# Kernel tuning notes

Measured on AMD Instinct MI355X. Metric: run time of the kernel, lower is better.

The kernel has to match this reference:

```python
import jax, jax.numpy as jnp
import numpy as np

C_IN, C_OUT, KH, KW = 64, 128, 3, 3
STRIDE, PAD, DIL = 1, 1, 1
EPS = 1e-5


def setup_inputs() -> dict:
    key = jax.random.key(0)
    ks = jax.random.split(key, 7)
    B, H, W = 8, 112, 112
    x = jax.random.normal(ks[0], (B, C_IN, H, W), dtype=jnp.float32)
    # offset conv: produces 2*KH*KW offset channels; small init keeps offsets sane
    w_off = jax.random.normal(ks[1], (2 * KH * KW, C_IN, KH, KW), dtype=jnp.float32) * 0.01
    b_off = jax.random.normal(ks[2], (2 * KH * KW,), dtype=jnp.float32) * 0.01
    # deformable conv weight/bias
    fan_in = C_IN * KH * KW
    w_dcn = jax.random.normal(ks[3], (C_OUT, C_IN, KH, KW), dtype=jnp.float32) / np.sqrt(fan_in)
    b_dcn = jax.random.normal(ks[4], (C_OUT,), dtype=jnp.float32) * 0.01
    gamma = jnp.ones((C_OUT,), dtype=jnp.float32)
    beta = jnp.zeros((C_OUT,), dtype=jnp.float32)
    return {"x": x, "w_off": w_off, "b_off": b_off, "w_dcn": w_dcn,
            "b_dcn": b_dcn, "gamma": gamma, "beta": beta}


def _conv2d(x, w, b):
    y = jax.lax.conv_general_dilated(
        x, w, window_strides=(STRIDE, STRIDE),
        padding=((PAD, PAD), (PAD, PAD)),
        rhs_dilation=(DIL, DIL),
        dimension_numbers=("NCHW", "OIHW", "NCHW"))
    return y + b[None, :, None, None]


def _deform_conv(x, offset, w, b):
    # x: [B,C,H,W]; offset: [B, 2*KH*KW, Ho, Wo] with (dy, dx) pairs per tap
    B, C, H, W = x.shape
    KK = KH * KW
    Ho, Wo = offset.shape[2], offset.shape[3]
    off = offset.reshape(B, KK, 2, Ho, Wo)
    ky = (jnp.arange(KK) // KW).astype(jnp.float32)  # kernel row per tap
    kx = (jnp.arange(KK) % KW).astype(jnp.float32)
    base_y = (jnp.arange(Ho) * STRIDE - PAD).astype(jnp.float32)
    base_x = (jnp.arange(Wo) * STRIDE - PAD).astype(jnp.float32)
    # sampling positions [B, KK, Ho, Wo]
    py = off[:, :, 0] + base_y[None, None, :, None] + (ky * DIL)[None, :, None, None]
    px = off[:, :, 1] + base_x[None, None, None, :] + (kx * DIL)[None, :, None, None]

    y0 = jnp.floor(py)
    x0 = jnp.floor(px)
    wy1 = py - y0  # weight for y0+1
    wx1 = px - x0
    y0i = y0.astype(jnp.int32)
    x0i = x0.astype(jnp.int32)

    x_flat = x.reshape(B, C, H * W)

    def gather_corner(yi, xi, wgt):
        # yi, xi, wgt: [B, KK, Ho, Wo]
        valid = (yi >= 0) & (yi < H) & (xi >= 0) & (xi < W)
        idx = jnp.clip(yi, 0, H - 1) * W + jnp.clip(xi, 0, W - 1)
        idx = idx.reshape(B, -1)  # [B, KK*Ho*Wo]
        vals = jnp.take_along_axis(x_flat, idx[:, None, :], axis=2)  # [B, C, N]
        coef = (wgt * valid.astype(wgt.dtype)).reshape(B, 1, -1)
        return vals * coef

    samp = (gather_corner(y0i,     x0i,     (1 - wy1) * (1 - wx1))
            + gather_corner(y0i,     x0i + 1, (1 - wy1) * wx1)
            + gather_corner(y0i + 1, x0i,     wy1 * (1 - wx1))
            + gather_corner(y0i + 1, x0i + 1, wy1 * wx1))
    samp = samp.reshape(B, C, KK, Ho, Wo)
    out = jnp.einsum("bckhw,ock->bohw", samp, w.reshape(w.shape[0], C, KK))
    return out + b[None, :, None, None]


def reference(x, w_off, b_off, w_dcn, b_dcn, gamma, beta):
    offset = _conv2d(x, w_off, b_off)
    y = _deform_conv(x, offset, w_dcn, b_dcn)
    # BatchNorm2d (training mode: biased batch stats) + ReLU
    mean = jnp.mean(y, axis=(0, 2, 3))
    var = jnp.var(y, axis=(0, 2, 3))
    yhat = (y - mean[None, :, None, None]) * jax.lax.rsqrt(var + EPS)[None, :, None, None]
    y = gamma[None, :, None, None] * yhat + beta[None, :, None, None]
    return jax.nn.relu(y)
```

## Files before the change

kernel.cpp:

```cpp
#include <hip/hip_runtime.h>

#define H    112
#define W    112
#define HW   12544
#define CIN  64
#define COUT 128
#define BATCH 8
#define KK   9
#define OFFC 18
#define EPS  1e-5f
#define TP   32
#define KDIM 576
#define KHALF 288
#define KPAD2 296
#define NB   3136
#define YST  40

typedef unsigned short ushort;
typedef unsigned int uint;
typedef __attribute__((ext_vector_type(8))) short short8;
typedef __attribute__((ext_vector_type(4))) float floatx4;
typedef __attribute__((ext_vector_type(2))) float f32x2;

__device__ __forceinline__ ushort f2bf(float f) {
  uint u = __float_as_uint(f);
  u = (u + 0x7FFFu + ((u >> 16) & 1u)) >> 16;
  return (ushort)u;
}

__device__ __forceinline__ uint pack_bf2(float f0, float f1) {
  uint u0 = __float_as_uint(f0) + 0x8000u;
  uint u1 = __float_as_uint(f1) + 0x8000u;
  return __builtin_amdgcn_perm(u1, u0, 0x07060302u);
}

__device__ __forceinline__ f32x2 up2(uint u) {
  f32x2 r;
  r.x = __uint_as_float(u << 16);
  r.y = __uint_as_float(u & 0xFFFF0000u);
  return r;
}

__global__ __launch_bounds__(256) void k_prep(
    const float* __restrict__ x, const float* __restrict__ w_off,
    const float* __restrict__ w_dcn, ushort* __restrict__ xTb,
    ushort* __restrict__ w_offT, ushort* __restrict__ w_mf) {
  if (blockIdx.y < BATCH) {
    __shared__ float tile[64][65];
    int b = blockIdx.y;
    int p0 = blockIdx.x * 64;
    int tid = threadIdx.x;
    int j = tid & 63, cb = tid >> 6;
#pragma unroll
    for (int i = 0; i < 16; ++i) {
      int ci = cb * 16 + i;
      tile[ci][j] = x[((size_t)(b * CIN + ci)) * HW + p0 + j];
    }
    __syncthreads();
    int px = tid >> 2, ciq = tid & 3;
#pragma unroll
    for (int g = 0; g < 4; ++g) {
      int ci = ciq * 16 + g * 4;
      uint lo = pack_bf2(tile[ci + 0][px], tile[ci + 1][px]);
      uint hi = pack_bf2(tile[ci + 2][px], tile[ci + 3][px]);
      *(uint2*)&xTb[((size_t)b * HW + p0 + px) * 64 + ci] = make_uint2(lo, hi);
    }
  } else {
    const int TOT = 32 * KDIM + COUT * KDIM;
    for (int i = blockIdx.x * 256 + threadIdx.x; i < TOT; i += 196 * 256) {
      if (i < 32 * KDIM) {
        int oc = i / KDIM, k = i - oc * KDIM;
        int kk = k >> 6, ci = k & 63;
        float v = (oc < OFFC) ? w_off[(oc * CIN + ci) * KK + kk] : 0.f;
        w_offT[i] = f2bf(v);
      } else {
        int jj = i - 32 * KDIM;
        int co = jj / KDIM, k = jj - co * KDIM;
        int h2 = k / KHALF, r = k - h2 * KHALF;
        int kk = r >> 5, cil = r & 31;
        int ci = h2 * 32 + cil;
        w_mf[jj] = f2bf(w_dcn[(co * CIN + ci) * KK + kk]);
      }
    }
  }
}

__global__ __launch_bounds__(256, 6) void k_deform(
    const ushort* __restrict__ xTb, const ushort* __restrict__ w_offT,
    const float* __restrict__ b_off, const ushort* __restrict__ w_mf,
    ushort* __restrict__ y, float* __restrict__ psT) {
  __shared__ float4  s_w[KK][TP];
  __shared__ ushort4 s_ip[KK][TP];
  __shared__ __align__(16) char smem_raw[TP * KPAD2 * 2];
  ushort (*samp)[KPAD2] = (ushort(*)[KPAD2])smem_raw;
  float  (*off_lds)[TP] = (float (*)[TP])smem_raw;

  int b = blockIdx.y;
  int p0 = blockIdx.x * TP;
  int bid = blockIdx.y * gridDim.x + blockIdx.x;
  int tid = threadIdx.x;
  const ushort* xb = xTb + (size_t)b * HW * 64;

  int wave = tid >> 6, lane = tid & 63;
  int row16 = lane & 15, quad = lane >> 4;

  {
    int pxblk = wave & 1, ocblk = wave >> 1;
    int pxl = pxblk * 16 + row16;
    int p = p0 + pxl;
    int ho = p / W, wo = p - ho * W;
    const ushort* wa = w_offT + (size_t)(ocblk * 16 + row16) * KDIM + quad * 8;
    floatx4 oacc = {0.f, 0.f, 0.f, 0.f};
#pragma unroll
    for (int ks = 0; ks < 18; ++ks) {
      int kk = ks >> 1;
      int ci0 = (ks & 1) * 32 + quad * 8;
      int kh = kk / 3, kw = kk - kh * 3;
      int yy = ho + kh - 1, xx = wo + kw - 1;
      short8 bv = {0, 0, 0, 0, 0, 0, 0, 0};
      if (yy >= 0 && yy < H && xx >= 0 && xx < W)
        bv = *(const short8*)(xb + ((size_t)(yy * W + xx) << 6) + ci0);
      short8 av = *(const short8*)(wa + ks * 32);
      oacc = __builtin_amdgcn_mfma_f32_16x16x32_bf16(av, bv, oacc, 0, 0, 0);
    }
#pragma unroll
    for (int reg = 0; reg < 4; ++reg) {
      int oc = ocblk * 16 + quad * 4 + reg;
      if (oc < OFFC) off_lds[oc][pxl] = oacc[reg] + b_off[oc];
    }
  }
  __syncthreads();

  for (int it = tid; it < KK * TP; it += 256) {
    int kk = it >> 5;
    int px = it & 31;
    int p = p0 + px;
    int ho = p / W, wo = p - ho * W;
    float dy = off_lds[2 * kk][px];
    float dx = off_lds[2 * kk + 1][px];
    float py = dy + (float)(ho - 1 + kk / 3);
    float pxx = dx + (float)(wo - 1 + kk % 3);
    float y0f = floorf(py), x0f = floorf(pxx);
    float wy1 = py - y0f, wx1 = pxx - x0f;
    int y0 = (int)y0f, x0 = (int)x0f;
    int y1 = y0 + 1, x1 = x0 + 1;
    float vy0 = (y0 >= 0 && y0 < H) ? 1.f : 0.f;
    float vy1 = (y1 >= 0 && y1 < H) ? 1.f : 0.f;
    float vx0 = (x0 >= 0 && x0 < W) ? 1.f : 0.f;
    float vx1 = (x1 >= 0 && x1 < W) ? 1.f : 0.f;
    int cy0 = min(max(y0, 0), H - 1), cy1 = min(max(y1, 0), H - 1);
    int cx0 = min(max(x0, 0), W - 1), cx1 = min(max(x1, 0), W - 1);
    s_w[kk][px] = make_float4((1.f - wy1) * (1.f - wx1) * vy0 * vx0,
                              (1.f - wy1) * wx1 * vy0 * vx1,
                              wy1 * (1.f - wx1) * vy1 * vx0,
                              wy1 * wx1 * vy1 * vx1);
    s_ip[kk][px] = make_ushort4((ushort)(cy0 * W + cx0), (ushort)(cy0 * W + cx1),
                                (ushort)(cy1 * W + cx0), (ushort)(cy1 * W + cx1));
  }
  __syncthreads();

  int koff = quad * 8;
  int co_base = wave * 32;
  const ushort* wa0 = w_mf + (size_t)(co_base + row16) * KDIM + koff;
  const ushort* wa1 = w_mf + (size_t)(co_base + 16 + row16) * KDIM + koff;

  floatx4 acc00 = {0.f, 0.f, 0.f, 0.f}, acc01 = acc00, acc10 = acc00, acc11 = acc00;

  for (int h = 0; h < 2; ++h) {
#pragma unroll
    for (int r = 0; r < 5; ++r) {
      int it = tid + r * 256;
      if (it < KK * TP * 4) {
        int kk = it >> 7;
        int px = (it >> 2) & 31;
        int cig = it & 3;
        int cil0 = cig * 8;
        int cio = h * 32 + cil0;
        float4 wv = s_w[kk][px];
        ushort4 ip = s_ip[kk][px];
        const ushort* g0 = xb + (((int)ip.x) << 6) + cio;
        const ushort* g1 = xb + (((int)ip.y) << 6) + cio;
        const ushort* g2 = xb + (((int)ip.z) << 6) + cio;
        const ushort* g3 = xb + (((int)ip.w) << 6) + cio;
        uint4 c0 = *(const uint4*)g0;
        uint4 c1 = *(const uint4*)g1;
        uint4 c2 = *(const uint4*)g2;
        uint4 c3 = *(const uint4*)g3;
        f32x2 r0 = up2(c0.x) * wv.x + up2(c1.x) * wv.y + up2(c2.x) * wv.z + up2(c3.x) * wv.w;
        f32x2 r1 = up2(c0.y) * wv.x + up2(c1.y) * wv.y + up2(c2.y) * wv.z + up2(c3.y) * wv.w;
        f32x2 r2 = up2(c0.z) * wv.x + up2(c1.z) * wv.y + up2(c2.z) * wv.z + up2(c3.z) * wv.w;
        f32x2 r3 = up2(c0.w) * wv.x + up2(c1.w) * wv.y + up2(c2.w) * wv.z + up2(c3.w) * wv.w;
        *(uint4*)&samp[px][kk * 32 + cil0] =
            make_uint4(pack_bf2(r0.x, r0.y), pack_bf2(r1.x, r1.y),
                       pack_bf2(r2.x, r2.y), pack_bf2(r3.x, r3.y));
      }
    }
    __syncthreads();

    const ushort* sb0 = &samp[row16][koff];
    const ushort* sb1 = &samp[16 + row16][koff];
    const ushort* a0 = wa0 + h * KHALF;
    const ushort* a1 = wa1 + h * KHALF;
#pragma unroll
    for (int ks = 0; ks < 9; ++ks) {
      short8 A0 = *(const short8*)(a0 + ks * 32);
      short8 A1 = *(const short8*)(a1 + ks * 32);
      short8 B0 = *(const short8*)(sb0 + ks * 32);
      short8 B1 = *(const short8*)(sb1 + ks * 32);
      acc00 = __builtin_amdgcn_mfma_f32_16x16x32_bf16(A0, B0, acc00, 0, 0, 0);
      acc01 = __builtin_amdgcn_mfma_f32_16x16x32_bf16(A0, B1, acc01, 0, 0, 0);
      acc10 = __builtin_amdgcn_mfma_f32_16x16x32_bf16(A1, B0, acc10, 0, 0, 0);
      acc11 = __builtin_amdgcn_mfma_f32_16x16x32_bf16(A1, B1, acc11, 0, 0, 0);
    }
    __syncthreads();
  }

  ushort (*yst)[YST] = (ushort(*)[YST])smem_raw;
#pragma unroll
  for (int reg = 0; reg < 4; ++reg) {
    int r0 = quad * 4 + reg;
    yst[co_base + r0][row16]            = f2bf(acc00[reg]);
    yst[co_base + r0][16 + row16]       = f2bf(acc01[reg]);
    yst[co_base + 16 + r0][row16]       = f2bf(acc10[reg]);
    yst[co_base + 16 + r0][16 + row16]  = f2bf(acc11[reg]);
  }
#pragma unroll
  for (int reg = 0; reg < 4; ++reg) {
    float s0 = acc00[reg] + acc01[reg];
    float q0 = acc00[reg] * acc00[reg] + acc01[reg] * acc01[reg];
    float s1 = acc10[reg] + acc11[reg];
    float q1 = acc10[reg] * acc10[reg] + acc11[reg] * acc11[reg];
#pragma unroll
    for (int m = 1; m < 16; m <<= 1) {
      s0 += __shfl_xor(s0, m, 64);
      q0 += __shfl_xor(q0, m, 64);
      s1 += __shfl_xor(s1, m, 64);
      q1 += __shfl_xor(q1, m, 64);
    }
    if (row16 == 0) {
      int c0 = co_base + quad * 4 + reg;
      float* pb = psT + (size_t)bid * 256;
      pb[c0] = s0;
      pb[COUT + c0] = q0;
      pb[c0 + 16] = s1;
      pb[COUT + c0 + 16] = q1;
    }
  }
  __syncthreads();
  {
    int co = tid >> 1, hf = tid & 1;
    const ushort* src = &yst[co][hf * 16];
    uint4 v0 = *(const uint4*)src;
    uint4 v1 = *(const uint4*)(src + 8);
    ushort* dst = y + (size_t)b * COUT * HW + (size_t)co * HW + p0 + hf * 16;
    *(uint4*)dst = v0;
    *(uint4*)(dst + 8) = v1;
  }
}

__global__ __launch_bounds__(256) void k_reduce(const float* __restrict__ psT,
                                                float* __restrict__ stats) {
  int c = threadIdx.x;
  float s = 0.f;
  for (int r = blockIdx.x; r < NB; r += gridDim.x)
    s += psT[(size_t)r * 256 + c];
  atomicAdd(&stats[c], s);
}

__global__ __launch_bounds__(256) void k_norm(const ushort* __restrict__ y,
                                              const float* __restrict__ stats,
                                              const float* __restrict__ gamma,
                                              const float* __restrict__ beta,
                                              float* __restrict__ out) {
  int i4 = blockIdx.x * 256 + threadIdx.x;
  const int total4 = BATCH * COUT * HW / 4;
  if (i4 >= total4) return;
  size_t i = (size_t)i4 * 4;
  int c = (int)((i / HW) & (COUT - 1));
  const float N = (float)(BATCH * HW);
  float m = stats[c] / N;
  float var = stats[COUT + c] / N - m * m;
  float r = rsqrtf(var + EPS);
  float g = gamma[c], bt = beta[c];
  uint2 u = *(const uint2*)&y[i];
  float4 v = make_float4(__uint_as_float(u.x << 16), __uint_as_float(u.x & 0xFFFF0000u),
                         __uint_as_float(u.y << 16), __uint_as_float(u.y & 0xFFFF0000u));
  v.x = fmaxf(0.f, (v.x - m) * r * g + bt);
  v.y = fmaxf(0.f, (v.y - m) * r * g + bt);
  v.z = fmaxf(0.f, (v.z - m) * r * g + bt);
  v.w = fmaxf(0.f, (v.w - m) * r * g + bt);
  *(float4*)&out[i] = v;
}

extern "C" void kernel_launch(void* const* d_in, const int* in_sizes, int n_in,
                              void* d_out, int out_size, void* d_ws, size_t ws_size,
                              hipStream_t stream) {
  const float* x     = (const float*)d_in[0];
  const float* w_off = (const float*)d_in[1];
  const float* b_off = (const float*)d_in[2];
  const float* w_dcn = (const float*)d_in[3];
  const float* gamma = (const float*)d_in[5];
  const float* beta  = (const float*)d_in[6];
  float* out = (float*)d_out;

  float* ws = (float*)d_ws;
  float*  psT    = ws;
  float*  stats  = psT + 802816;
  ushort* xTb    = (ushort*)(stats + 256);
  ushort* w_mf   = xTb + (size_t)BATCH * HW * 64;
  ushort* w_offT = w_mf + COUT * KDIM;
  ushort* y_bf   = w_offT + 32 * KDIM;

  hipMemsetAsync(stats, 0, 256 * sizeof(float), stream);
  k_prep<<<dim3(196, 9), 256, 0, stream>>>(x, w_off, w_dcn, xTb, w_offT, w_mf);
  k_deform<<<dim3(HW / TP, BATCH), 256, 0, stream>>>(xTb, w_offT, b_off, w_mf, y_bf, psT);
  k_reduce<<<32, 256, 0, stream>>>(psT, stats);
  k_norm<<<BATCH * COUT * HW / 4 / 256, 256, 0, stream>>>(y_bf, stats, gamma, beta, out);
}
```

Baseline: 254.4 us.

## Split offset conv into separate kernel and use padded atomics for BN stats

The offset convolution moves out of the deform kernel into its own MFMA kernel that writes offsets to a global buffer, and the deform kernel reads them from there. BN partial sums are now accumulated with atomics into a stats array padded to 16 floats per channel, which removes the per-block partials buffer and the separate reduce kernel. Zeroing of the stats moves into the prep kernel, replacing the memset. This shortens the deform kernel and removes a launch, but adds an extra global round trip for the offsets and many contended atomics.

```diff
diff --git a/kernel.cpp b/kernel.cpp
--- a/kernel.cpp
+++ b/kernel.cpp
@@ -15,6 +15,7 @@
 #define KPAD2 296
 #define NB   3136
 #define YST  40
+#define SSTRIDE 16
 
 typedef unsigned short ushort;
 typedef unsigned int uint;
@@ -44,7 +45,8 @@
 __global__ __launch_bounds__(256) void k_prep(
     const float* __restrict__ x, const float* __restrict__ w_off,
     const float* __restrict__ w_dcn, ushort* __restrict__ xTb,
-    ushort* __restrict__ w_offT, ushort* __restrict__ w_mf) {
+    ushort* __restrict__ w_offT, ushort* __restrict__ w_mf,
+    float* __restrict__ stats) {
   if (blockIdx.y < BATCH) {
     __shared__ float tile[64][65];
     int b = blockIdx.y;
@@ -66,8 +68,13 @@
       *(uint2*)&xTb[((size_t)b * HW + p0 + px) * 64 + ci] = make_uint2(lo, hi);
     }
   } else {
+    int tid = threadIdx.x;
+    if (blockIdx.x == 0) {
+#pragma unroll
+      for (int i = tid; i < 256 * SSTRIDE; i += 256) stats[i] = 0.f;
+    }
     const int TOT = 32 * KDIM + COUT * KDIM;
-    for (int i = blockIdx.x * 256 + threadIdx.x; i < TOT; i += 196 * 256) {
+    for (int i = blockIdx.x * 256 + tid; i < TOT; i += 196 * 256) {
       if (i < 32 * KDIM) {
         int oc = i / KDIM, k = i - oc * KDIM;
         int kk = k >> 6, ci = k & 63;
@@ -85,59 +92,69 @@
   }
 }
 
+__global__ __launch_bounds__(256) void k_offset_conv(
+    const ushort* __restrict__ xTb, const ushort* __restrict__ w_offT,
+    const float* __restrict__ bias, float* __restrict__ out) {
+  int b = blockIdx.y;
+  int wave = threadIdx.x >> 6, lane = threadIdx.x & 63;
+  int row16 = lane & 15, quad = lane >> 4;
+  int p = blockIdx.x * 64 + wave * 16 + row16;
+  int ho = p / W, wo = p - ho * W;
+  const ushort* xb = xTb + (size_t)b * HW * 64;
+
+  short8 Bf[18];
+#pragma unroll
+  for (int ks = 0; ks < 18; ++ks) {
+    int kk = ks >> 1;
+    int ci0 = (ks & 1) * 32 + quad * 8;
+    int kh = kk / 3, kw = kk - kh * 3;
+    int yy = ho + kh - 1, xx = wo + kw - 1;
+    bool valid = (yy >= 0) & (yy < H) & (xx >= 0) & (xx < W);
+    short8 v = {0, 0, 0, 0, 0, 0, 0, 0};
+    if (valid) v = *(const short8*)(xb + ((size_t)(yy * W + xx) << 6) + ci0);
+    Bf[ks] = v;
+  }
+  floatx4 acc0 = {0.f, 0.f, 0.f, 0.f}, acc1 = acc0;
+  const ushort* wa0 = w_offT + row16 * KDIM + quad * 8;
+  const ushort* wa1 = w_offT + (16 + row16) * KDIM + quad * 8;
+#pragma unroll
+  for (int ks = 0; ks < 18; ++ks) {
+    short8 A0 = *(const short8*)(wa0 + ks * 32);
+    short8 A1 = *(const short8*)(wa1 + ks * 32);
+    acc0 = __builtin_amdgcn_mfma_f32_16x16x32_bf16(A0, Bf[ks], acc0, 0, 0, 0);
+    acc1 = __builtin_amdgcn_mfma_f32_16x16x32_bf16(A1, Bf[ks], acc1, 0, 0, 0);
+  }
+  float* ob = out + (size_t)b * OFFC * HW;
+#pragma unroll
+  for (int reg = 0; reg < 4; ++reg) {
+    int oc = quad * 4 + reg;
+    ob[(size_t)oc * HW + p] = acc0[reg] + bias[oc];
+    int oc1 = 16 + oc;
+    if (oc1 < OFFC) ob[(size_t)oc1 * HW + p] = acc1[reg] + bias[oc1];
+  }
+}
+
 __global__ __launch_bounds__(256, 6) void k_deform(
-    const ushort* __restrict__ xTb, const ushort* __restrict__ w_offT,
-    const float* __restrict__ b_off, const ushort* __restrict__ w_mf,
-    ushort* __restrict__ y, float* __restrict__ psT) {
+    const ushort* __restrict__ xTb, const float* __restrict__ off,
+    const ushort* __restrict__ w_mf, ushort* __restrict__ y,
+    float* __restrict__ stats) {
   __shared__ float4  s_w[KK][TP];
   __shared__ ushort4 s_ip[KK][TP];
   __shared__ __align__(16) char smem_raw[TP * KPAD2 * 2];
   ushort (*samp)[KPAD2] = (ushort(*)[KPAD2])smem_raw;
-  float  (*off_lds)[TP] = (float (*)[TP])smem_raw;
 
   int b = blockIdx.y;
   int p0 = blockIdx.x * TP;
-  int bid = blockIdx.y * gridDim.x + blockIdx.x;
   int tid = threadIdx.x;
   const ushort* xb = xTb + (size_t)b * HW * 64;
-
-  int wave = tid >> 6, lane = tid & 63;
-  int row16 = lane & 15, quad = lane >> 4;
-
-  {
-    int pxblk = wave & 1, ocblk = wave >> 1;
-    int pxl = pxblk * 16 + row16;
-    int p = p0 + pxl;
-    int ho = p / W, wo = p - ho * W;
-    const ushort* wa = w_offT + (size_t)(ocblk * 16 + row16) * KDIM + quad * 8;
-    floatx4 oacc = {0.f, 0.f, 0.f, 0.f};
-#pragma unroll
-    for (int ks = 0; ks < 18; ++ks) {
-      int kk = ks >> 1;
-      int ci0 = (ks & 1) * 32 + quad * 8;
-      int kh = kk / 3, kw = kk - kh * 3;
-      int yy = ho + kh - 1, xx = wo + kw - 1;
-      short8 bv = {0, 0, 0, 0, 0, 0, 0, 0};
-      if (yy >= 0 && yy < H && xx >= 0 && xx < W)
-        bv = *(const short8*)(xb + ((size_t)(yy * W + xx) << 6) + ci0);
-      short8 av = *(const short8*)(wa + ks * 32);
-      oacc = __builtin_amdgcn_mfma_f32_16x16x32_bf16(av, bv, oacc, 0, 0, 0);
-    }
-#pragma unroll
-    for (int reg = 0; reg < 4; ++reg) {
-      int oc = ocblk * 16 + quad * 4 + reg;
-      if (oc < OFFC) off_lds[oc][pxl] = oacc[reg] + b_off[oc];
-    }
-  }
-  __syncthreads();
 
   for (int it = tid; it < KK * TP; it += 256) {
     int kk = it >> 5;
     int px = it & 31;
     int p = p0 + px;
     int ho = p / W, wo = p - ho * W;
-    float dy = off_lds[2 * kk][px];
-    float dx = off_lds[2 * kk + 1][px];
+    float dy = off[((size_t)b * OFFC + 2 * kk) * HW + p];
+    float dx = off[((size_t)b * OFFC + 2 * kk + 1) * HW + p];
     float py = dy + (float)(ho - 1 + kk / 3);
     float pxx = dx + (float)(wo - 1 + kk % 3);
     float y0f = floorf(py), x0f = floorf(pxx);
@@ -159,6 +176,8 @@
   }
   __syncthreads();
 
+  int wave = tid >> 6, lane = tid & 63;
+  int row16 = lane & 15, quad = lane >> 4;
   int koff = quad * 8;
   int co_base = wave * 32;
   const ushort* wa0 = w_mf + (size_t)(co_base + row16) * KDIM + koff;
@@ -239,11 +258,11 @@
     }
     if (row16 == 0) {
       int c0 = co_base + quad * 4 + reg;
-      float* pb = psT + (size_t)bid * 256;
-      pb[c0] = s0;
-      pb[COUT + c0] = q0;
-      pb[c0 + 16] = s1;
-      pb[COUT + c0 + 16] = q1;
+      int c1 = c0 + 16;
+      atomicAdd(&stats[(size_t)c0 * SSTRIDE], s0);
+      atomicAdd(&stats[(size_t)(128 + c0) * SSTRIDE], q0);
+      atomicAdd(&stats[(size_t)c1 * SSTRIDE], s1);
+      atomicAdd(&stats[(size_t)(128 + c1) * SSTRIDE], q1);
     }
   }
   __syncthreads();
@@ -256,15 +275,6 @@
     *(uint4*)dst = v0;
     *(uint4*)(dst + 8) = v1;
   }
-}
-
-__global__ __launch_bounds__(256) void k_reduce(const float* __restrict__ psT,
-                                                float* __restrict__ stats) {
-  int c = threadIdx.x;
-  float s = 0.f;
-  for (int r = blockIdx.x; r < NB; r += gridDim.x)
-    s += psT[(size_t)r * 256 + c];
-  atomicAdd(&stats[c], s);
 }
 
 __global__ __launch_bounds__(256) void k_norm(const ushort* __restrict__ y,
@@ -278,8 +288,8 @@
   size_t i = (size_t)i4 * 4;
   int c = (int)((i / HW) & (COUT - 1));
   const float N = (float)(BATCH * HW);
-  float m = stats[c] / N;
-  float var = stats[COUT + c] / N - m * m;
+  float m = stats[(size_t)c * SSTRIDE] / N;
+  float var = stats[(size_t)(COUT + c) * SSTRIDE] / N - m * m;
   float r = rsqrtf(var + EPS);
   float g = gamma[c], bt = beta[c];
   uint2 u = *(const uint2*)&y[i];
@@ -304,16 +314,15 @@
   float* out = (float*)d_out;
 
   float* ws = (float*)d_ws;
-  float*  psT    = ws;
-  float*  stats  = psT + 802816;
-  ushort* xTb    = (ushort*)(stats + 256);
-  ushort* w_mf   = xTb + (size_t)BATCH * HW * 64;
-  ushort* w_offT = w_mf + COUT * KDIM;
-  ushort* y_bf   = w_offT + 32 * KDIM;
-
-  hipMemsetAsync(stats, 0, 256 * sizeof(float), stream);
-  k_prep<<<dim3(196, 9), 256, 0, stream>>>(x, w_off, w_dcn, xTb, w_offT, w_mf);
-  k_deform<<<dim3(HW / TP, BATCH), 256, 0, stream>>>(xTb, w_offT, b_off, w_mf, y_bf, psT);
-  k_reduce<<<32, 256, 0, stream>>>(psT, stats);
+  float*  off_buf = ws;
+  float*  stats   = off_buf + 1806336;
+  ushort* xTb     = (ushort*)(stats + 256 * SSTRIDE);
+  ushort* w_mf    = xTb + (size_t)BATCH * HW * 64;
+  ushort* w_offT  = w_mf + COUT * KDIM;
+  ushort* y_bf    = w_offT + 32 * KDIM;
+
+  k_prep<<<dim3(196, 9), 256, 0, stream>>>(x, w_off, w_dcn, xTb, w_offT, w_mf, stats);
+  k_offset_conv<<<dim3(HW / 64, BATCH), 256, 0, stream>>>(xTb, w_offT, b_off, off_buf);
+  k_deform<<<dim3(HW / TP, BATCH), 256, 0, stream>>>(xTb, off_buf, w_mf, y_bf, stats);
   k_norm<<<BATCH * COUT * HW / 4 / 256, 256, 0, stream>>>(y_bf, stats, gamma, beta, out);
 }
```

New measurement: 259.0 us. About the same (+1.8%).
